# Optimization experiments

Hardware: AMD Instinct MI355X
Metric: run time of the kernel (lower is better)

## Reference

```python
import jax, jax.numpy as jnp
import numpy as np

N_NODES = 100000
N_EDGES = 1600000
IN_C, HID_C, OUT_C = 128, 128, 64


def gcn_conv(x, src, dst, n_nodes, W, b):
    # PyG GCNConv (normalize=True, add_self_loops=True):
    # out = D^{-1/2} (A+I) D^{-1/2} (x @ W^T) + b
    h = x @ W.T                                   # [N, out]
    deg = jax.ops.segment_sum(jnp.ones(src.shape, x.dtype), dst,
                              num_segments=n_nodes)  # includes self-loops
    dinv = jnp.where(deg > 0, jax.lax.rsqrt(deg), 0.0)
    norm = dinv[src] * dinv[dst]                  # [E+N]
    msg = h[src] * norm[:, None]                  # gather + scale
    out = jax.ops.segment_sum(msg, dst, num_segments=n_nodes)
    return out + b


def setup_inputs() -> dict:
    key = jax.random.key(0)
    ks = jax.random.split(key, 8)
    x = jax.random.normal(ks[0], (N_NODES, IN_C), dtype=jnp.float32)
    edge_index = jax.random.randint(ks[1], (2, N_EDGES), 0, N_NODES, dtype=jnp.int64)

    def lin(k, fan_out, fan_in):
        s = 1.0 / np.sqrt(fan_in)
        kw, kb = jax.random.split(k)
        W = jax.random.uniform(kw, (fan_out, fan_in), jnp.float32, -s, s)
        b = jax.random.uniform(kb, (fan_out,), jnp.float32, -s, s)
        return W, b

    W1, b1 = lin(ks[2], HID_C, IN_C)
    W2, b2 = lin(ks[3], HID_C, HID_C)
    W3, b3 = lin(ks[4], OUT_C, HID_C)
    return {"x": x, "edge_index": edge_index,
            "W1": W1, "b1": b1, "W2": W2, "b2": b2, "W3": W3, "b3": b3}


def reference(x, edge_index, W1, b1, W2, b2, W3, b3):
    n = x.shape[0]
    loop = jnp.arange(n, dtype=edge_index.dtype)
    src = jnp.concatenate([edge_index[0], loop])  # add self-loops once; identical per layer
    dst = jnp.concatenate([edge_index[1], loop])
    h = gcn_conv(x, src, dst, n, W1, b1)
    h = jax.nn.relu(h)
    h = gcn_conv(h, src, dst, n, W2, b2)
    h = jax.nn.relu(h)
    h = gcn_conv(h, src, dst, n, W3, b3)
    return h
```

## Files before the change

### kernel.cpp

```cpp
#include <hip/hip_runtime.h>


#define NPB 256
#define CAP 4672
#define BIN_WGS 512

typedef short bfrag __attribute__((ext_vector_type(8)));
typedef float f32x4 __attribute__((ext_vector_type(4)));
typedef unsigned short u16x8 __attribute__((ext_vector_type(8)));

__global__ __launch_bounds__(256) void bin_edges(const int* __restrict__ src,
                                                 const int* __restrict__ dst,
                                                 int* __restrict__ cur,
                                                 int* __restrict__ binned,
                                                 int E, int B) {
  __shared__ int lc[512];
  __shared__ int lbase[512];
  const int t = threadIdx.x;
  const int chunk = (E + BIN_WGS - 1) / BIN_WGS;
  const int e0 = blockIdx.x * chunk;
  const int e1 = min(E, e0 + chunk);

  for (int i = t; i < B; i += 256) lc[i] = 0;
  __syncthreads();
  for (int e = e0 + t; e < e1; e += 256) {
    int d = dst[e];
    atomicAdd(&lc[d >> 8], 1);
  }
  __syncthreads();
  for (int i = t; i < B; i += 256) {
    int c = lc[i];
    lbase[i] = c ? atomicAdd(&cur[i], c) : 0;
    lc[i] = 0;
  }
  __syncthreads();
  for (int e = e0 + t; e < e1; e += 256) {
    int d = dst[e];
    int s = __builtin_nontemporal_load(&src[e]);
    int bk = d >> 8;
    int p = lbase[bk] + atomicAdd(&lc[bk], 1);
    if (p < (bk + 1) * CAP)
      binned[p] = ((d & 255) << 24) | s;
  }
}

__global__ __launch_bounds__(256) void build_buckets(const int* __restrict__ binned,
                                                     const int* __restrict__ cur,
                                                     int* __restrict__ cols,
                                                     int2* __restrict__ off2,
                                                     float* __restrict__ dinv,
                                                     int N) {
  __shared__ int eb[CAP];
  __shared__ int ob[CAP];
  __shared__ int lc[256];
  __shared__ int sc[256];
  const int b = blockIdx.x;
  const int t = threadIdx.x;
  const int base = b * CAP;
  const int cntb = min(cur[b] - base, CAP);

  for (int i = t; i < cntb; i += 256) eb[i] = binned[base + i];
  lc[t] = 0;
  __syncthreads();
  for (int i = t; i < cntb; i += 256)
    atomicAdd(&lc[(unsigned)eb[i] >> 24], 1);
  __syncthreads();
  int myc = lc[t];
  sc[t] = myc;
  __syncthreads();
  for (int d = 1; d < 256; d <<= 1) {
    int a = (t >= d) ? sc[t - d] : 0;
    __syncthreads();
    sc[t] += a;
    __syncthreads();
  }
  int excl = sc[t] - myc;
  int node = b * NPB + t;
  if (node < N) {
    off2[node] = make_int2(base + excl, base + excl + myc);
    dinv[node] = rsqrtf((float)(myc + 1));
  }
  lc[t] = excl;
  __syncthreads();
  for (int i = t; i < cntb; i += 256) {
    int e = eb[i];
    int p = atomicAdd(&lc[(unsigned)e >> 24], 1);
    ob[p] = e & 0xFFFFFF;
  }
  __syncthreads();
  for (int i = t; i < cntb; i += 256) cols[base + i] = ob[i];
}

__device__ inline unsigned short bf16rne(float x) {
  unsigned u = __float_as_uint(x);
  return (unsigned short)((u + 0x7FFFu + ((u >> 16) & 1u)) >> 16);
}
__device__ inline float bf16lo(unsigned q) { return __uint_as_float(q << 16); }
__device__ inline float bf16hi(unsigned q) { return __uint_as_float(q & 0xFFFF0000u); }

__global__ __launch_bounds__(256) void split_w3(const float* __restrict__ W1,
                                                const float* __restrict__ W2,
                                                const float* __restrict__ W3,
                                                unsigned short* __restrict__ w1h,
                                                unsigned short* __restrict__ w1l,
                                                unsigned short* __restrict__ w2h,
                                                unsigned short* __restrict__ w2l,
                                                unsigned short* __restrict__ w3h,
                                                unsigned short* __restrict__ w3l,
                                                int* __restrict__ cur, int B) {
  int i = blockIdx.x * 256 + threadIdx.x;
  const float* W;
  unsigned short *hi, *lo;
  int j;
  if (i < 16384) {
    W = W1; hi = w1h; lo = w1l; j = i;
  } else if (i < 32768) {
    W = W2; hi = w2h; lo = w2l; j = i - 16384;
  } else if (i < 40960) {
    W = W3; hi = w3h; lo = w3l; j = i - 32768;
  } else if (i < 40960 + B) {
    cur[i - 40960] = (i - 40960) * CAP;
    return;
  } else {
    return;
  }
  float v = W[j];
  unsigned short h = bf16rne(v);
  hi[j] = h;
  lo[j] = bf16rne(v - __uint_as_float((unsigned)h << 16));
}

#define LDP 136

template <int OUTC>
__global__ __launch_bounds__(256) void gemm_planes(const unsigned short* __restrict__ Xh,
                                                   const unsigned short* __restrict__ Xl,
                                                   const unsigned short* __restrict__ Whg,
                                                   const unsigned short* __restrict__ Wlg,
                                                   const float* __restrict__ dinv,
                                                   unsigned short* __restrict__ Y,
                                                   int M) {
  constexpr int CHUNKS = OUTC / 64;
  __shared__ unsigned short Whi[64 * LDP], Wlo[64 * LDP];
  const int tid = threadIdx.x;
  const int m_base = blockIdx.x * 64;
  const int lane = tid & 63;
  const int wv = tid >> 6;
  const int col_l = lane & 15;
  const int quad = lane >> 4;
  const size_t arow = (size_t)min(m_base + wv * 16 + col_l, M - 1) * 128;
  const int bBase = col_l * LDP + quad * 8;

  bfrag aH[4], aL[4];
#pragma unroll
  for (int ks = 0; ks < 4; ++ks) {
    aH[ks] = *(const bfrag*)(Xh + arow + ks * 32 + quad * 8);
    aL[ks] = *(const bfrag*)(Xl + arow + ks * 32 + quad * 8);
  }

  f32x4 acc[CHUNKS][4];
#pragma unroll
  for (int c2 = 0; c2 < CHUNKS; ++c2)
#pragma unroll
    for (int t = 0; t < 4; ++t) acc[c2][t] = {0.f, 0.f, 0.f, 0.f};

#pragma unroll
  for (int c2 = 0; c2 < CHUNKS; ++c2) {
    if (c2) __syncthreads();
    for (int idx = tid; idx < 64 * 16; idx += 256) {
      int r = idx >> 4, g = idx & 15;
      *(u16x8*)(Whi + r * LDP + g * 8) =
          *(const u16x8*)(Whg + (size_t)(c2 * 64 + r) * 128 + g * 8);
      *(u16x8*)(Wlo + r * LDP + g * 8) =
          *(const u16x8*)(Wlg + (size_t)(c2 * 64 + r) * 128 + g * 8);
    }
    __syncthreads();
#pragma unroll
    for (int ks = 0; ks < 4; ++ks) {
#pragma unroll
      for (int t = 0; t < 4; ++t) {
        int bo = bBase + t * 16 * LDP + ks * 32;
        bfrag bHi = *(const bfrag*)(Whi + bo);
        bfrag bLo = *(const bfrag*)(Wlo + bo);
        acc[c2][t] = __builtin_amdgcn_mfma_f32_16x16x32_bf16(aH[ks], bHi, acc[c2][t], 0, 0, 0);
        acc[c2][t] = __builtin_amdgcn_mfma_f32_16x16x32_bf16(aL[ks], bHi, acc[c2][t], 0, 0, 0);
        acc[c2][t] = __builtin_amdgcn_mfma_f32_16x16x32_bf16(aH[ks], bLo, acc[c2][t], 0, 0, 0);
      }
    }
  }

#pragma unroll
  for (int r = 0; r < 4; ++r) {
    int row = m_base + wv * 16 + quad * 4 + r;
    if (row < M) {
      float s = dinv[row];
#pragma unroll
      for (int c2 = 0; c2 < CHUNKS; ++c2)
#pragma unroll
        for (int t = 0; t < 4; ++t) {
          unsigned short h = bf16rne(acc[c2][t][r] * s);
          Y[(size_t)row * OUTC + c2 * 64 + t * 16 + col_l] = h;
        }
    }
  }
}

template <int OUTC>
__global__ __launch_bounds__(256) void gemm_xsplit(const float* __restrict__ X,
                                                   const unsigned short* __restrict__ Whg,
                                                   const unsigned short* __restrict__ Wlg,
                                                   const float* __restrict__ dinv,
                                                   unsigned short* __restrict__ Y,
                                                   int M) {
  constexpr int CHUNKS = OUTC / 64;
  __shared__ unsigned short Whi[64 * LDP], Wlo[64 * LDP];
  const int tid = threadIdx.x;
  const int m_base = blockIdx.x * 64;
  const int lane = tid & 63;
  const int wv = tid >> 6;
  const int col_l = lane & 15;
  const int quad = lane >> 4;
  const size_t arow = (size_t)min(m_base + wv * 16 + col_l, M - 1) * 128;
  const int bBase = col_l * LDP + quad * 8;

  bfrag aH[4], aL[4];
#pragma unroll
  for (int ks = 0; ks < 4; ++ks) {
    float4 v0 = *(const float4*)(X + arow + ks * 32 + quad * 8);
    float4 v1 = *(const float4*)(X + arow + ks * 32 + quad * 8 + 4);
    float vv[8] = {v0.x, v0.y, v0.z, v0.w, v1.x, v1.y, v1.z, v1.w};
#pragma unroll
    for (int j = 0; j < 8; ++j) {
      unsigned short h = bf16rne(vv[j]);
      aH[ks][j] = (short)h;
      aL[ks][j] = (short)bf16rne(vv[j] - __uint_as_float((unsigned)h << 16));
    }
  }

  f32x4 acc[CHUNKS][4];
#pragma unroll
  for (int c2 = 0; c2 < CHUNKS; ++c2)
#pragma unroll
    for (int t = 0; t < 4; ++t) acc[c2][t] = {0.f, 0.f, 0.f, 0.f};

#pragma unroll
  for (int c2 = 0; c2 < CHUNKS; ++c2) {
    if (c2) __syncthreads();
    for (int idx = tid; idx < 64 * 16; idx += 256) {
      int r = idx >> 4, g = idx & 15;
      *(u16x8*)(Whi + r * LDP + g * 8) =
          *(const u16x8*)(Whg + (size_t)(c2 * 64 + r) * 128 + g * 8);
      *(u16x8*)(Wlo + r * LDP + g * 8) =
          *(const u16x8*)(Wlg + (size_t)(c2 * 64 + r) * 128 + g * 8);
    }
    __syncthreads();
#pragma unroll
    for (int ks = 0; ks < 4; ++ks) {
#pragma unroll
      for (int t = 0; t < 4; ++t) {
        int bo = bBase + t * 16 * LDP + ks * 32;
        bfrag bHi = *(const bfrag*)(Whi + bo);
        bfrag bLo = *(const bfrag*)(Wlo + bo);
        acc[c2][t] = __builtin_amdgcn_mfma_f32_16x16x32_bf16(aH[ks], bHi, acc[c2][t], 0, 0, 0);
        acc[c2][t] = __builtin_amdgcn_mfma_f32_16x16x32_bf16(aL[ks], bHi, acc[c2][t], 0, 0, 0);
        acc[c2][t] = __builtin_amdgcn_mfma_f32_16x16x32_bf16(aH[ks], bLo, acc[c2][t], 0, 0, 0);
      }
    }
  }

#pragma unroll
  for (int r = 0; r < 4; ++r) {
    int row = m_base + wv * 16 + quad * 4 + r;
    if (row < M) {
      float s = dinv[row];
#pragma unroll
      for (int c2 = 0; c2 < CHUNKS; ++c2)
#pragma unroll
        for (int t = 0; t < 4; ++t) {
          unsigned short h = bf16rne(acc[c2][t][r] * s);
          Y[(size_t)row * OUTC + c2 * 64 + t * 16 + col_l] = h;
        }
    }
  }
}

__device__ inline void acc_add(float* a, uint4 d) {
  a[0] += bf16lo(d.x); a[1] += bf16hi(d.x);
  a[2] += bf16lo(d.y); a[3] += bf16hi(d.y);
  a[4] += bf16lo(d.z); a[5] += bf16hi(d.z);
  a[6] += bf16lo(d.w); a[7] += bf16hi(d.w);
}

template <int C, bool RELU, bool SPLIT>
__global__ __launch_bounds__(256) void aggregate4(const unsigned short* __restrict__ xs,
                                                  const int2* __restrict__ off2,
                                                  const int* __restrict__ cols,
                                                  const float* __restrict__ dinv,
                                                  const float* __restrict__ bias,
                                                  float* __restrict__ outf,
                                                  unsigned short* __restrict__ oh,
                                                  unsigned short* __restrict__ ol,
                                                  int N) {
  constexpr int GL = C / 8;
  constexpr int LSH = (GL == 16) ? 4 : 3;
  constexpr int NPBk = 256 / GL;
  const int t = threadIdx.x;
  const int gl = t & (GL - 1);
  const int node = blockIdx.x * NPBk + (t >> LSH);
  if (node >= N) return;

  const unsigned co = (unsigned)gl * 16;
  const char* xb = (const char*)xs;

  float acc[8];
  {
    uint4 d = *(const uint4*)(xb + (size_t)node * (C * 2) + co);
    acc[0] = bf16lo(d.x); acc[1] = bf16hi(d.x);
    acc[2] = bf16lo(d.y); acc[3] = bf16hi(d.y);
    acc[4] = bf16lo(d.z); acc[5] = bf16hi(d.z);
    acc[6] = bf16lo(d.w); acc[7] = bf16hi(d.w);
  }

  const int2 oo = off2[node];
  const int en = oo.y;
  for (int e0 = oo.x; e0 < en; e0 += GL) {
    int col = __builtin_nontemporal_load(&cols[min(e0 + gl, en - 1)]);
    int m = en - e0;
    if (m > GL) m = GL;
    const int c1 = m - 1;
    for (int j = 0; j < m; j += 4) {
      int s0 = __shfl(col, min(j,     c1), GL);
      int s1 = __shfl(col, min(j + 1, c1), GL);
      int s2 = __shfl(col, min(j + 2, c1), GL);
      int s3 = __shfl(col, min(j + 3, c1), GL);
      uint4 d0 = *(const uint4*)(xb + (size_t)s0 * (C * 2) + co);
      uint4 d1 = *(const uint4*)(xb + (size_t)s1 * (C * 2) + co);
      uint4 d2 = *(const uint4*)(xb + (size_t)s2 * (C * 2) + co);
      uint4 d3 = *(const uint4*)(xb + (size_t)s3 * (C * 2) + co);
      acc_add(acc, d0);
      if (j + 1 < m) acc_add(acc, d1);
      if (j + 2 < m) acc_add(acc, d2);
      if (j + 3 < m) acc_add(acc, d3);
    }
  }

  const float dd = dinv[node];
  const float4 bA = *(const float4*)(bias + gl * 8);
  const float4 bB = *(const float4*)(bias + gl * 8 + 4);
  float h[8];
  h[0] = acc[0] * dd + bA.x; h[1] = acc[1] * dd + bA.y;
  h[2] = acc[2] * dd + bA.z; h[3] = acc[3] * dd + bA.w;
  h[4] = acc[4] * dd + bB.x; h[5] = acc[5] * dd + bB.y;
  h[6] = acc[6] * dd + bB.z; h[7] = acc[7] * dd + bB.w;
  if (RELU) {
#pragma unroll
    for (int q = 0; q < 8; ++q) h[q] = fmaxf(h[q], 0.f);
  }
  if (SPLIT) {
    u16x8 hv, lv;
#pragma unroll
    for (int q = 0; q < 8; ++q) {
      unsigned short hb = bf16rne(h[q]);
      hv[q] = hb;
      lv[q] = bf16rne(h[q] - __uint_as_float((unsigned)hb << 16));
    }
    __builtin_nontemporal_store(hv, (u16x8*)(oh + (size_t)node * C + gl * 8));
    __builtin_nontemporal_store(lv, (u16x8*)(ol + (size_t)node * C + gl * 8));
  } else {
    f32x4 oA = {h[0], h[1], h[2], h[3]};
    f32x4 oB = {h[4], h[5], h[6], h[7]};
    __builtin_nontemporal_store(oA, (f32x4*)(outf + (size_t)node * C + gl * 8));
    __builtin_nontemporal_store(oB, (f32x4*)(outf + (size_t)node * C + gl * 8 + 4));
  }
}


extern "C" void kernel_launch(void* const* d_in, const int* in_sizes, int n_in,
                              void* d_out, int out_size, void* d_ws, size_t ws_size,
                              hipStream_t stream) {
  const float* x  = (const float*)d_in[0];
  const int*   ei = (const int*)d_in[1];
  const float* W1 = (const float*)d_in[2];
  const float* b1 = (const float*)d_in[3];
  const float* W2 = (const float*)d_in[4];
  const float* b2 = (const float*)d_in[5];
  const float* W3 = (const float*)d_in[6];
  const float* b3 = (const float*)d_in[7];

  const int N = in_sizes[0] / 128;
  const int E = in_sizes[1] / 2;
  const int* src = ei;
  const int* dst = ei + E;
  const int B = (N + NPB - 1) / NPB;

  char* w = (char*)d_ws;
  size_t p = 0;
  auto alloc = [&](size_t bytes) -> void* {
    void* r = w + p;
    p = (p + bytes + 255) & ~(size_t)255;
    return r;
  };
  float*    dinv   = (float*)alloc((size_t)N * 4);
  int2*     off2   = (int2*)alloc((size_t)N * 8);
  int*      cur    = (int*)alloc((size_t)B * 4);
  int*      binned = (int*)alloc((size_t)B * CAP * 4);
  int*      cols   = (int*)alloc((size_t)B * CAP * 4);
  unsigned short* xsb = (unsigned short*)alloc((size_t)N * 128 * 2);
  unsigned short* hh  = (unsigned short*)alloc((size_t)N * 128 * 2);
  unsigned short* hl  = (unsigned short*)alloc((size_t)N * 128 * 2);
  unsigned short* w1h = (unsigned short*)alloc(128 * 128 * 2);
  unsigned short* w1l = (unsigned short*)alloc(128 * 128 * 2);
  unsigned short* w2h = (unsigned short*)alloc(128 * 128 * 2);
  unsigned short* w2l = (unsigned short*)alloc(128 * 128 * 2);
  unsigned short* w3h = (unsigned short*)alloc(64 * 128 * 2);
  unsigned short* w3l = (unsigned short*)alloc(64 * 128 * 2);

  split_w3<<<(40960 + B + 255) / 256, 256, 0, stream>>>(W1, W2, W3, w1h, w1l,
                                                        w2h, w2l, w3h, w3l,
                                                        cur, B);
  bin_edges<<<BIN_WGS, 256, 0, stream>>>(src, dst, cur, binned, E, B);
  build_buckets<<<B, 256, 0, stream>>>(binned, cur, cols, off2, dinv, N);

  const int gb = (N + 63) / 64;
  const int ab128 = (N + 15) / 16;
  const int ab64  = (N + 31) / 32;

  gemm_xsplit<128><<<gb, 256, 0, stream>>>(x, w1h, w1l, dinv, xsb, N);
  aggregate4<128, true, true><<<ab128, 256, 0, stream>>>(xsb, off2, cols, dinv, b1,
                                                         nullptr, hh, hl, N);
  gemm_planes<128><<<gb, 256, 0, stream>>>(hh, hl, w2h, w2l, dinv, xsb, N);
  aggregate4<128, true, true><<<ab128, 256, 0, stream>>>(xsb, off2, cols, dinv, b2,
                                                         nullptr, hh, hl, N);
  gemm_planes<64><<<gb, 256, 0, stream>>>(hh, hl, w3h, w3l, dinv, xsb, N);
  aggregate4<64, false, false><<<ab64, 256, 0, stream>>>(xsb, off2, cols, dinv, b3,
                                                         (float*)d_out, nullptr,
                                                         nullptr, N);
}
```

Measured before the change: 379.0 us.

## Split 128-channel aggregation into 32-byte channel slices across blocks

Adds an aggregation kernel for the two 128-channel layers that assigns each block one 16-channel slice (32 bytes) for 128 nodes, with two lanes per node. The blockIdx layout interleaves the eight channel groups of a node tile, so consecutive blocks read the same neighbour rows and may hit in L2. The aim is to get more nodes in flight per wave and more memory-level parallelism for the irregular gathers. In exchange, the edge column indices are re-read once per channel group (eight times), and each gather moves only 32 bytes per row, which may waste cache-line bandwidth.

```diff
diff --git a/kernel.cpp b/kernel.cpp
--- a/kernel.cpp
+++ b/kernel.cpp
@@ -291,6 +291,77 @@
   a[6] += bf16lo(d.w); a[7] += bf16hi(d.w);
 }
 
+__global__ __launch_bounds__(256) void aggregate_cs(const unsigned short* __restrict__ xs,
+                                                    const int2* __restrict__ off2,
+                                                    const int* __restrict__ cols,
+                                                    const float* __restrict__ dinv,
+                                                    const float* __restrict__ bias,
+                                                    unsigned short* __restrict__ oh,
+                                                    unsigned short* __restrict__ ol,
+                                                    int N) {
+  const int cg = blockIdx.x & 7;
+  const int tile = blockIdx.x >> 3;
+  const int t = threadIdx.x;
+  const int gl = t & 1;
+  const int node = tile * 128 + (t >> 1);
+  if (node >= N) return;
+
+  const unsigned co = (unsigned)cg * 32 + (unsigned)gl * 16;
+  const char* xb = (const char*)xs;
+
+  float acc[8];
+  {
+    uint4 d = *(const uint4*)(xb + (size_t)node * 256 + co);
+    acc[0] = bf16lo(d.x); acc[1] = bf16hi(d.x);
+    acc[2] = bf16lo(d.y); acc[3] = bf16hi(d.y);
+    acc[4] = bf16lo(d.z); acc[5] = bf16hi(d.z);
+    acc[6] = bf16lo(d.w); acc[7] = bf16hi(d.w);
+  }
+
+  const int2 oo = off2[node];
+  const int en = oo.y;
+  for (int e0 = oo.x; e0 < en; e0 += 4) {
+    int ca = __builtin_nontemporal_load(&cols[min(e0 + gl * 2,     en - 1)]);
+    int cb = __builtin_nontemporal_load(&cols[min(e0 + gl * 2 + 1, en - 1)]);
+    int m = en - e0;
+    if (m > 4) m = 4;
+    int s0 = __shfl(ca, 0, 2);
+    int s1 = __shfl(cb, 0, 2);
+    int s2 = __shfl(ca, 1, 2);
+    int s3 = __shfl(cb, 1, 2);
+    uint4 d0 = *(const uint4*)(xb + (size_t)s0 * 256 + co);
+    uint4 d1 = *(const uint4*)(xb + (size_t)s1 * 256 + co);
+    uint4 d2 = *(const uint4*)(xb + (size_t)s2 * 256 + co);
+    uint4 d3 = *(const uint4*)(xb + (size_t)s3 * 256 + co);
+    acc_add(acc, d0);
+    if (m > 1) acc_add(acc, d1);
+    if (m > 2) acc_add(acc, d2);
+    if (m > 3) acc_add(acc, d3);
+  }
+
+  const float dd = dinv[node];
+  const float4 bA = *(const float4*)(bias + cg * 16 + gl * 8);
+  const float4 bB = *(const float4*)(bias + cg * 16 + gl * 8 + 4);
+  float h[8];
+  h[0] = acc[0] * dd + bA.x; h[1] = acc[1] * dd + bA.y;
+  h[2] = acc[2] * dd + bA.z; h[3] = acc[3] * dd + bA.w;
+  h[4] = acc[4] * dd + bB.x; h[5] = acc[5] * dd + bB.y;
+  h[6] = acc[6] * dd + bB.z; h[7] = acc[7] * dd + bB.w;
+#pragma unroll
+  for (int q = 0; q < 8; ++q) h[q] = fmaxf(h[q], 0.f);
+
+  u16x8 hv, lv;
+#pragma unroll
+  for (int q = 0; q < 8; ++q) {
+    unsigned short hb = bf16rne(h[q]);
+    hv[q] = hb;
+    lv[q] = bf16rne(h[q] - __uint_as_float((unsigned)hb << 16));
+  }
+  const size_t ob = (size_t)node * 128 + cg * 16 + gl * 8;
+  __builtin_nontemporal_store(hv, (u16x8*)(oh + ob));
+  __builtin_nontemporal_store(lv, (u16x8*)(ol + ob));
+}
+
 template <int C, bool RELU, bool SPLIT>
 __global__ __launch_bounds__(256) void aggregate4(const unsigned short* __restrict__ xs,
                                                   const int2* __restrict__ off2,
@@ -422,15 +493,13 @@
   build_buckets<<<B, 256, 0, stream>>>(binned, cur, cols, off2, dinv, N);
 
   const int gb = (N + 63) / 64;
-  const int ab128 = (N + 15) / 16;
-  const int ab64  = (N + 31) / 32;
+  const int acs = ((N + 127) / 128) * 8;
+  const int ab64 = (N + 31) / 32;
 
   gemm_xsplit<128><<<gb, 256, 0, stream>>>(x, w1h, w1l, dinv, xsb, N);
-  aggregate4<128, true, true><<<ab128, 256, 0, stream>>>(xsb, off2, cols, dinv, b1,
-                                                         nullptr, hh, hl, N);
+  aggregate_cs<<<acs, 256, 0, stream>>>(xsb, off2, cols, dinv, b1, hh, hl, N);
   gemm_planes<128><<<gb, 256, 0, stream>>>(hh, hl, w2h, w2l, dinv, xsb, N);
-  aggregate4<128, true, true><<<ab128, 256, 0, stream>>>(xsb, off2, cols, dinv, b2,
-                                                         nullptr, hh, hl, N);
+  aggregate_cs<<<acs, 256, 0, stream>>>(xsb, off2, cols, dinv, b2, hh, hl, N);
   gemm_planes<64><<<gb, 256, 0, stream>>>(hh, hl, w3h, w3l, dinv, xsb, N);
   aggregate4<64, false, false><<<ab64, 256, 0, stream>>>(xsb, off2, cols, dinv, b3,
                                                          (float*)d_out, nullptr,
```

New measurement: 705.1 us. 86.0% more time.
